# Kernel tuning notes

Measured on AMD Instinct MI355X. Metric: run time of the kernel, lower is better.

## Reference

```python
import jax, jax.numpy as jnp
import numpy as np

# Dims: batch=64, n_cols=512, n_e=80, n_i=20, embed=512
DT_OVER_TAU = 0.1  # leaky rate-neuron integration constant (dt/tau)

B, C, NE, NI, E = 64, 512, 80, 20, 512


def setup_inputs() -> dict:
    key = jax.random.key(0)
    ks = jax.random.split(key, 12)
    return {
        "thal": jax.random.normal(ks[0], (B, E), jnp.float32),
        "thal_increments": jax.random.normal(ks[1], (B, C, E), jnp.float32),
        "l23_fb": jax.random.normal(ks[2], (B, C, NE), jnp.float32),
        # state (rates nonnegative, membrane potentials gaussian)
        "r_e": jax.random.uniform(ks[3], (B, C, NE), jnp.float32),
        "r_i": jax.random.uniform(ks[4], (B, C, NI), jnp.float32),
        "e_v": jax.random.normal(ks[5], (B, C, NE), jnp.float32),
        "i_v": jax.random.normal(ks[6], (B, C, NI), jnp.float32),
        # learned params (per-column weight stacks)
        "input_proj": jax.random.normal(ks[7], (C, NE, E), jnp.float32) * (1.0 / np.sqrt(E).astype(np.float32)),
        "feedback_proj": jax.random.normal(ks[8], (C, NE, NE), jnp.float32) * (1.0 / np.sqrt(NE).astype(np.float32)),
        # static synapses: nonnegative weights, sign handled by E/I convention
        "W_ee": jax.random.uniform(ks[9], (C, NE, NE), jnp.float32) * (1.0 / np.sqrt(NE).astype(np.float32)),
        "W_ei": jax.random.uniform(ks[10], (C, NI, NE), jnp.float32) * (1.0 / np.sqrt(NE).astype(np.float32)),
        "W_ie": jax.random.uniform(ks[11], (C, NE, NI), jnp.float32) * (1.0 / np.sqrt(NI).astype(np.float32)),
    }


def reference(thal, thal_increments, l23_fb, r_e, r_i, e_v, i_v,
              input_proj, feedback_proj, W_ee, W_ei, W_ie):
    # thal [B,E] broadcast over columns + per-column increments -> [B,C,E]
    thal_full = thal[:, None, :] + thal_increments
    # external + feedback drive onto excitatory pop: [B,C,NE]
    I_ext = jnp.einsum('bce,coe->bco', thal_full, input_proj)
    I_fb = jnp.einsum('bce,coe->bco', l23_fb, feedback_proj)
    # synapse currents (static weights; E->E, E->I excitatory, I->E inhibitory)
    I_ee = jnp.einsum('bcp,cop->bco', r_e, W_ee)   # [B,C,NE]
    I_ei = jnp.einsum('bcp,cop->bco', r_e, W_ei)   # [B,C,NI]
    I_ie = -jnp.einsum('bcp,cop->bco', r_i, W_ie)  # [B,C,NE], inhibitory
    I_e_total = I_ext + I_fb + I_ee + I_ie
    I_i_total = I_ei
    # leaky rate-neuron state update: v <- v + dt/tau * (-v + I); r = relu(v)
    v_e_new = e_v + DT_OVER_TAU * (I_e_total - e_v)
    v_i_new = i_v + DT_OVER_TAU * (I_i_total - i_v)
    r_e_new = jax.nn.relu(v_e_new)
    r_i_new = jax.nn.relu(v_i_new)
    # (layer_outputs e_out/l23_out/l5_out all alias r_e_new; return new state too)
    return r_e_new, r_i_new, v_e_new, v_i_new
```

## Files before the change

### kernel.cpp

```cpp
#include <hip/hip_runtime.h>


typedef unsigned int u32;

__global__ __launch_bounds__(256) void ei_cols_f32(
    const float* __restrict__ thal,
    const float* __restrict__ inc,
    const float* __restrict__ l23,
    const float* __restrict__ re_in,
    const float* __restrict__ ri_in,
    const float* __restrict__ ev_in,
    const float* __restrict__ iv_in,
    const float* __restrict__ in_proj,
    const float* __restrict__ fb_proj,
    const float* __restrict__ w_ee,
    const float* __restrict__ w_ei,
    const float* __restrict__ w_ie,
    float* __restrict__ out)
{
  __shared__ __align__(16) float smem[14784];
  const int c = blockIdx.x;
  const int tid = threadIdx.x;
  const int tx = tid & 15;
  const int ty = tid >> 4;

  float acc_e[4][5];
  float acc_i[4][2];
#pragma unroll
  for (int ib = 0; ib < 4; ++ib) {
#pragma unroll
    for (int io = 0; io < 5; ++io) acc_e[ib][io] = 0.f;
    acc_i[ib][0] = 0.f;
    acc_i[ib][1] = 0.f;
  }

  {
    float* As = smem;
    float* Ws = smem + 4352;
    for (int k0 = 0; k0 < 512; k0 += 64) {
      __syncthreads();
      for (int l = tid; l < 1024; l += 256) {
        int b = l >> 4, kk = (l & 15) << 2;
        float4 tv = *(const float4*)(thal + b * 512 + k0 + kk);
        float4 iv = *(const float4*)(inc + (size_t)b * 262144 + (size_t)c * 512 + k0 + kk);
        float4 s;
        s.x = tv.x + iv.x; s.y = tv.y + iv.y; s.z = tv.z + iv.z; s.w = tv.w + iv.w;
        *(float4*)(As + b * 68 + kk) = s;
      }
      for (int l = tid; l < 1280; l += 256) {
        int o = l >> 4, kk = (l & 15) << 2;
        *(float4*)(Ws + o * 68 + kk) =
            *(const float4*)(in_proj + (size_t)c * 40960 + o * 512 + k0 + kk);
      }
      __syncthreads();
#pragma unroll 4
      for (int kc = 0; kc < 64; kc += 4) {
        float4 av[4], wv[5];
#pragma unroll
        for (int ib = 0; ib < 4; ++ib)
          av[ib] = *(const float4*)(As + (ty + 16 * ib) * 68 + kc);
#pragma unroll
        for (int io = 0; io < 5; ++io)
          wv[io] = *(const float4*)(Ws + (tx + 16 * io) * 68 + kc);
#pragma unroll
        for (int ib = 0; ib < 4; ++ib)
#pragma unroll
          for (int io = 0; io < 5; ++io) {
            float a = acc_e[ib][io];
            a = fmaf(av[ib].x, wv[io].x, a);
            a = fmaf(av[ib].y, wv[io].y, a);
            a = fmaf(av[ib].z, wv[io].z, a);
            a = fmaf(av[ib].w, wv[io].w, a);
            acc_e[ib][io] = a;
          }
      }
    }
  }

  {
    __syncthreads();
    float* As = smem;
    float* Bs = smem + 5376;
    for (int l = tid; l < 1280; l += 256) {
      int b = l / 20, kk = (l % 20) << 2;
      *(float4*)(As + b * 84 + kk) =
          *(const float4*)(l23 + ((size_t)b * 512 + c) * 80 + kk);
    }
    for (int l = tid; l < 1600; l += 256) {
      int o = l / 20, kk = (l % 20) << 2;
      *(float4*)(Bs + o * 84 + kk) =
          *(const float4*)(fb_proj + ((size_t)c * 80 + o) * 80 + kk);
    }
    __syncthreads();
#pragma unroll 4
    for (int kc = 0; kc < 80; kc += 4) {
      float4 av[4], wv[5];
#pragma unroll
      for (int ib = 0; ib < 4; ++ib)
        av[ib] = *(const float4*)(As + (ty + 16 * ib) * 84 + kc);
#pragma unroll
      for (int io = 0; io < 5; ++io)
        wv[io] = *(const float4*)(Bs + (tx + 16 * io) * 84 + kc);
#pragma unroll
      for (int ib = 0; ib < 4; ++ib)
#pragma unroll
        for (int io = 0; io < 5; ++io) {
          float a = acc_e[ib][io];
          a = fmaf(av[ib].x, wv[io].x, a);
          a = fmaf(av[ib].y, wv[io].y, a);
          a = fmaf(av[ib].z, wv[io].z, a);
          a = fmaf(av[ib].w, wv[io].w, a);
          acc_e[ib][io] = a;
        }
    }
  }

  {
    __syncthreads();
    float* As = smem;
    float* W1 = smem + 5376;
    float* W2 = smem + 12096;
    for (int l = tid; l < 1280; l += 256) {
      int b = l / 20, kk = (l % 20) << 2;
      *(float4*)(As + b * 84 + kk) =
          *(const float4*)(re_in + ((size_t)b * 512 + c) * 80 + kk);
    }
    for (int l = tid; l < 1600; l += 256) {
      int o = l / 20, kk = (l % 20) << 2;
      *(float4*)(W1 + o * 84 + kk) =
          *(const float4*)(w_ee + ((size_t)c * 80 + o) * 80 + kk);
    }
    for (int l = tid; l < 640; l += 256) {
      int o = l / 20, kk = (l % 20) << 2;
      float4 v = {0.f, 0.f, 0.f, 0.f};
      if (o < 20) v = *(const float4*)(w_ei + ((size_t)c * 20 + o) * 80 + kk);
      *(float4*)(W2 + o * 84 + kk) = v;
    }
    __syncthreads();
#pragma unroll 4
    for (int kc = 0; kc < 80; kc += 4) {
      float4 av[4], wv[5], w2[2];
#pragma unroll
      for (int ib = 0; ib < 4; ++ib)
        av[ib] = *(const float4*)(As + (ty + 16 * ib) * 84 + kc);
#pragma unroll
      for (int io = 0; io < 5; ++io)
        wv[io] = *(const float4*)(W1 + (tx + 16 * io) * 84 + kc);
#pragma unroll
      for (int io = 0; io < 2; ++io)
        w2[io] = *(const float4*)(W2 + (tx + 16 * io) * 84 + kc);
#pragma unroll
      for (int ib = 0; ib < 4; ++ib) {
#pragma unroll
        for (int io = 0; io < 5; ++io) {
          float a = acc_e[ib][io];
          a = fmaf(av[ib].x, wv[io].x, a);
          a = fmaf(av[ib].y, wv[io].y, a);
          a = fmaf(av[ib].z, wv[io].z, a);
          a = fmaf(av[ib].w, wv[io].w, a);
          acc_e[ib][io] = a;
        }
#pragma unroll
        for (int io = 0; io < 2; ++io) {
          float a = acc_i[ib][io];
          a = fmaf(av[ib].x, w2[io].x, a);
          a = fmaf(av[ib].y, w2[io].y, a);
          a = fmaf(av[ib].z, w2[io].z, a);
          a = fmaf(av[ib].w, w2[io].w, a);
          acc_i[ib][io] = a;
        }
      }
    }
  }

  {
    __syncthreads();
    float* Ri = smem;
    float* Wn = smem + 1792;
    for (int l = tid; l < 320; l += 256) {
      int b = l / 5, kk = (l % 5) << 2;
      *(float4*)(Ri + b * 28 + kk) =
          *(const float4*)(ri_in + ((size_t)b * 512 + c) * 20 + kk);
    }
    for (int l = tid; l < 400; l += 256) {
      int o = l / 5, kk = (l % 5) << 2;
      float4 v = *(const float4*)(w_ie + ((size_t)c * 80 + o) * 20 + kk);
      v.x = -v.x; v.y = -v.y; v.z = -v.z; v.w = -v.w;
      *(float4*)(Wn + o * 28 + kk) = v;
    }
    __syncthreads();
#pragma unroll
    for (int kc = 0; kc < 20; kc += 4) {
      float4 av[4], wv[5];
#pragma unroll
      for (int ib = 0; ib < 4; ++ib)
        av[ib] = *(const float4*)(Ri + (ty + 16 * ib) * 28 + kc);
#pragma unroll
      for (int io = 0; io < 5; ++io)
        wv[io] = *(const float4*)(Wn + (tx + 16 * io) * 28 + kc);
#pragma unroll
      for (int ib = 0; ib < 4; ++ib)
#pragma unroll
        for (int io = 0; io < 5; ++io) {
          float a = acc_e[ib][io];
          a = fmaf(av[ib].x, wv[io].x, a);
          a = fmaf(av[ib].y, wv[io].y, a);
          a = fmaf(av[ib].z, wv[io].z, a);
          a = fmaf(av[ib].w, wv[io].w, a);
          acc_e[ib][io] = a;
        }
    }
  }

  const size_t R_ri = 2621440u;
  const size_t R_ve = 3276800u;
  const size_t R_vi = 5898240u;
#pragma unroll
  for (int ib = 0; ib < 4; ++ib) {
    int b = ty + 16 * ib;
#pragma unroll
    for (int io = 0; io < 5; ++io) {
      int o = tx + 16 * io;
      size_t g = ((size_t)b * 512 + c) * 80 + o;
      float ev = ev_in[g];
      float v = ev + 0.1f * (acc_e[ib][io] - ev);
      out[g] = fmaxf(v, 0.f);
      out[R_ve + g] = v;
    }
#pragma unroll
    for (int io = 0; io < 2; ++io) {
      int oi = tx + 16 * io;
      if (oi < 20) {
        size_t g = ((size_t)b * 512 + c) * 20 + oi;
        float iv = iv_in[g];
        float v = iv + 0.1f * (acc_i[ib][io] - iv);
        out[R_ri + g] = fmaxf(v, 0.f);
        out[R_vi + g] = v;
      }
    }
  }
}

extern "C" void kernel_launch(void* const* d_in, const int* in_sizes, int n_in,
                              void* d_out, int out_size, void* d_ws, size_t ws_size,
                              hipStream_t stream) {
  const float* thal = (const float*)d_in[0];
  const float* inc = (const float*)d_in[1];
  const float* l23 = (const float*)d_in[2];
  const float* re = (const float*)d_in[3];
  const float* ri = (const float*)d_in[4];
  const float* ev = (const float*)d_in[5];
  const float* iv = (const float*)d_in[6];
  const float* in_proj = (const float*)d_in[7];
  const float* fb_proj = (const float*)d_in[8];
  const float* w_ee = (const float*)d_in[9];
  const float* w_ei = (const float*)d_in[10];
  const float* w_ie = (const float*)d_in[11];
  float* out = (float*)d_out;
  ei_cols_f32<<<dim3(512), dim3(256), 0, stream>>>(
      thal, inc, l23, re, ri, ev, iv, in_proj, fb_proj, w_ee, w_ei, w_ie, out);
}
```

Before: 307.1 us.

## Switch per-column GEMMs to bf16 MFMA with register-prefetched double buffering

```diff
diff --git a/kernel.cpp b/kernel.cpp
--- a/kernel.cpp
+++ b/kernel.cpp
@@ -1,9 +1,26 @@
 #include <hip/hip_runtime.h>
-
-
+#include <hip/hip_bf16.h>
+
+typedef __attribute__((ext_vector_type(8))) short bf16x8;
+typedef __attribute__((ext_vector_type(4))) float f32x4;
+typedef unsigned short u16;
 typedef unsigned int u32;
 
-__global__ __launch_bounds__(256) void ei_cols_f32(
+__device__ __forceinline__ u16 f2bf(float f) {
+  __hip_bfloat16 h = __float2bfloat16(f);
+  u16 u;
+  __builtin_memcpy(&u, &h, 2);
+  return u;
+}
+__device__ __forceinline__ void cvt4_store(u16* dst, float4 v) {
+  u16 rr[4] = {f2bf(v.x), f2bf(v.y), f2bf(v.z), f2bf(v.w)};
+  uint2 p;
+  __builtin_memcpy(&p, rr, 8);
+  *(uint2*)dst = p;
+}
+
+
+__global__ __launch_bounds__(256) void ei_cols_mfma(
     const float* __restrict__ thal,
     const float* __restrict__ inc,
     const float* __restrict__ l23,
@@ -18,226 +35,248 @@
     const float* __restrict__ w_ie,
     float* __restrict__ out)
 {
-  __shared__ __align__(16) float smem[14784];
+  __shared__ __align__(16) unsigned char smem[41472];
   const int c = blockIdx.x;
   const int tid = threadIdx.x;
-  const int tx = tid & 15;
-  const int ty = tid >> 4;
-
-  float acc_e[4][5];
-  float acc_i[4][2];
-#pragma unroll
-  for (int ib = 0; ib < 4; ++ib) {
-#pragma unroll
-    for (int io = 0; io < 5; ++io) acc_e[ib][io] = 0.f;
-    acc_i[ib][0] = 0.f;
-    acc_i[ib][1] = 0.f;
-  }
+  const int lane = tid & 63;
+  const int wave = tid >> 6;
+  const int nidx = lane & 15;
+  const int quad = lane >> 4;
+  const int m0 = wave * 16;
+
+  f32x4 acc_e[5], acc_i[2];
+#pragma unroll
+  for (int j = 0; j < 5; ++j) acc_e[j] = (f32x4){0.f, 0.f, 0.f, 0.f};
+#pragma unroll
+  for (int j = 0; j < 2; ++j) acc_i[j] = (f32x4){0.f, 0.f, 0.f, 0.f};
 
   {
-    float* As = smem;
-    float* Ws = smem + 4352;
-    for (int k0 = 0; k0 < 512; k0 += 64) {
+    float4 tv[4], gv[4], wv[5];
+
+    auto load_regs = [&](int k0) {
+#pragma unroll
+      for (int j = 0; j < 4; ++j) {
+        int l = tid + j * 256;
+        int b = l >> 4, kk = (l & 15) << 2;
+        tv[j] = *(const float4*)(thal + b * 512 + k0 + kk);
+        gv[j] = *(const float4*)(inc + (size_t)b * 262144 + (size_t)c * 512 + k0 + kk);
+      }
+#pragma unroll
+      for (int j = 0; j < 5; ++j) {
+        int l = tid + j * 256;
+        int o = l >> 4, kk = (l & 15) << 2;
+        wv[j] = *(const float4*)(in_proj + (size_t)c * 40960 + o * 512 + k0 + kk);
+      }
+    };
+    auto store_buf = [&](int p) {
+      u16* A = (u16*)(smem + p * 20736);
+      u16* W = (u16*)(smem + 9216 + p * 20736);
+#pragma unroll
+      for (int j = 0; j < 4; ++j) {
+        int l = tid + j * 256;
+        int b = l >> 4, kk = (l & 15) << 2;
+        float4 s;
+        s.x = tv[j].x + gv[j].x; s.y = tv[j].y + gv[j].y;
+        s.z = tv[j].z + gv[j].z; s.w = tv[j].w + gv[j].w;
+        cvt4_store(A + b * 72 + kk, s);
+      }
+#pragma unroll
+      for (int j = 0; j < 5; ++j) {
+        int l = tid + j * 256;
+        int o = l >> 4, kk = (l & 15) << 2;
+        cvt4_store(W + o * 72 + kk, wv[j]);
+      }
+    };
+
+    load_regs(0);
+    store_buf(0);
+    for (int i = 0; i < 8; ++i) {
       __syncthreads();
-      for (int l = tid; l < 1024; l += 256) {
-        int b = l >> 4, kk = (l & 15) << 2;
-        float4 tv = *(const float4*)(thal + b * 512 + k0 + kk);
-        float4 iv = *(const float4*)(inc + (size_t)b * 262144 + (size_t)c * 512 + k0 + kk);
-        float4 s;
-        s.x = tv.x + iv.x; s.y = tv.y + iv.y; s.z = tv.z + iv.z; s.w = tv.w + iv.w;
-        *(float4*)(As + b * 68 + kk) = s;
-      }
-      for (int l = tid; l < 1280; l += 256) {
-        int o = l >> 4, kk = (l & 15) << 2;
-        *(float4*)(Ws + o * 68 + kk) =
-            *(const float4*)(in_proj + (size_t)c * 40960 + o * 512 + k0 + kk);
-      }
-      __syncthreads();
-#pragma unroll 4
-      for (int kc = 0; kc < 64; kc += 4) {
-        float4 av[4], wv[5];
-#pragma unroll
-        for (int ib = 0; ib < 4; ++ib)
-          av[ib] = *(const float4*)(As + (ty + 16 * ib) * 68 + kc);
-#pragma unroll
-        for (int io = 0; io < 5; ++io)
-          wv[io] = *(const float4*)(Ws + (tx + 16 * io) * 68 + kc);
-#pragma unroll
-        for (int ib = 0; ib < 4; ++ib)
-#pragma unroll
-          for (int io = 0; io < 5; ++io) {
-            float a = acc_e[ib][io];
-            a = fmaf(av[ib].x, wv[io].x, a);
-            a = fmaf(av[ib].y, wv[io].y, a);
-            a = fmaf(av[ib].z, wv[io].z, a);
-            a = fmaf(av[ib].w, wv[io].w, a);
-            acc_e[ib][io] = a;
-          }
-      }
+      if (i < 7) load_regs((i + 1) * 64);
+      const int p = i & 1;
+      u16* A = (u16*)(smem + p * 20736);
+      u16* W = (u16*)(smem + 9216 + p * 20736);
+#pragma unroll
+      for (int kk0 = 0; kk0 < 64; kk0 += 32) {
+        bf16x8 a = *(const bf16x8*)(A + (m0 + nidx) * 72 + kk0 + quad * 8);
+#pragma unroll
+        for (int j = 0; j < 5; ++j) {
+          bf16x8 b = *(const bf16x8*)(W + (j * 16 + nidx) * 72 + kk0 + quad * 8);
+          acc_e[j] = __builtin_amdgcn_mfma_f32_16x16x32_bf16(a, b, acc_e[j], 0, 0, 0);
+        }
+      }
+      if (i < 7) store_buf((i + 1) & 1);
     }
   }
 
   {
     __syncthreads();
-    float* As = smem;
-    float* Bs = smem + 5376;
+    u16* As = (u16*)smem;
+    u16* Bs = (u16*)(smem + 13312);
     for (int l = tid; l < 1280; l += 256) {
       int b = l / 20, kk = (l % 20) << 2;
-      *(float4*)(As + b * 84 + kk) =
-          *(const float4*)(l23 + ((size_t)b * 512 + c) * 80 + kk);
+      cvt4_store(As + b * 104 + kk,
+                 *(const float4*)(l23 + ((size_t)b * 512 + c) * 80 + kk));
+    }
+    for (int l = tid; l < 128; l += 256) {
+      int b = l >> 1, off = 80 + (l & 1) * 8;
+      *(uint4*)(As + b * 104 + off) = (uint4){0u, 0u, 0u, 0u};
     }
     for (int l = tid; l < 1600; l += 256) {
       int o = l / 20, kk = (l % 20) << 2;
-      *(float4*)(Bs + o * 84 + kk) =
-          *(const float4*)(fb_proj + ((size_t)c * 80 + o) * 80 + kk);
-    }
-    __syncthreads();
-#pragma unroll 4
-    for (int kc = 0; kc < 80; kc += 4) {
-      float4 av[4], wv[5];
-#pragma unroll
-      for (int ib = 0; ib < 4; ++ib)
-        av[ib] = *(const float4*)(As + (ty + 16 * ib) * 84 + kc);
-#pragma unroll
-      for (int io = 0; io < 5; ++io)
-        wv[io] = *(const float4*)(Bs + (tx + 16 * io) * 84 + kc);
-#pragma unroll
-      for (int ib = 0; ib < 4; ++ib)
-#pragma unroll
-        for (int io = 0; io < 5; ++io) {
-          float a = acc_e[ib][io];
-          a = fmaf(av[ib].x, wv[io].x, a);
-          a = fmaf(av[ib].y, wv[io].y, a);
-          a = fmaf(av[ib].z, wv[io].z, a);
-          a = fmaf(av[ib].w, wv[io].w, a);
-          acc_e[ib][io] = a;
-        }
+      cvt4_store(Bs + o * 104 + kk,
+                 *(const float4*)(fb_proj + ((size_t)c * 80 + o) * 80 + kk));
+    }
+    for (int l = tid; l < 160; l += 256) {
+      int o = l >> 1, off = 80 + (l & 1) * 8;
+      *(uint4*)(Bs + o * 104 + off) = (uint4){0u, 0u, 0u, 0u};
+    }
+    __syncthreads();
+#pragma unroll
+    for (int kk0 = 0; kk0 < 96; kk0 += 32) {
+      bf16x8 a = *(const bf16x8*)(As + (m0 + nidx) * 104 + kk0 + quad * 8);
+#pragma unroll
+      for (int j = 0; j < 5; ++j) {
+        bf16x8 b = *(const bf16x8*)(Bs + (j * 16 + nidx) * 104 + kk0 + quad * 8);
+        acc_e[j] = __builtin_amdgcn_mfma_f32_16x16x32_bf16(a, b, acc_e[j], 0, 0, 0);
+      }
     }
   }
 
   {
     __syncthreads();
-    float* As = smem;
-    float* W1 = smem + 5376;
-    float* W2 = smem + 12096;
+    u16* As = (u16*)smem;
+    u16* W1 = (u16*)(smem + 13312);
+    u16* W2 = (u16*)(smem + 29952);
     for (int l = tid; l < 1280; l += 256) {
       int b = l / 20, kk = (l % 20) << 2;
-      *(float4*)(As + b * 84 + kk) =
-          *(const float4*)(re_in + ((size_t)b * 512 + c) * 80 + kk);
+      cvt4_store(As + b * 104 + kk,
+                 *(const float4*)(re_in + ((size_t)b * 512 + c) * 80 + kk));
+    }
+    for (int l = tid; l < 128; l += 256) {
+      int b = l >> 1, off = 80 + (l & 1) * 8;
+      *(uint4*)(As + b * 104 + off) = (uint4){0u, 0u, 0u, 0u};
     }
     for (int l = tid; l < 1600; l += 256) {
       int o = l / 20, kk = (l % 20) << 2;
-      *(float4*)(W1 + o * 84 + kk) =
-          *(const float4*)(w_ee + ((size_t)c * 80 + o) * 80 + kk);
-    }
-    for (int l = tid; l < 640; l += 256) {
+      cvt4_store(W1 + o * 104 + kk,
+                 *(const float4*)(w_ee + ((size_t)c * 80 + o) * 80 + kk));
+    }
+    for (int l = tid; l < 160; l += 256) {
+      int o = l >> 1, off = 80 + (l & 1) * 8;
+      *(uint4*)(W1 + o * 104 + off) = (uint4){0u, 0u, 0u, 0u};
+    }
+    for (int l = tid; l < 400; l += 256) {
       int o = l / 20, kk = (l % 20) << 2;
-      float4 v = {0.f, 0.f, 0.f, 0.f};
-      if (o < 20) v = *(const float4*)(w_ei + ((size_t)c * 20 + o) * 80 + kk);
-      *(float4*)(W2 + o * 84 + kk) = v;
-    }
-    __syncthreads();
-#pragma unroll 4
-    for (int kc = 0; kc < 80; kc += 4) {
-      float4 av[4], wv[5], w2[2];
-#pragma unroll
-      for (int ib = 0; ib < 4; ++ib)
-        av[ib] = *(const float4*)(As + (ty + 16 * ib) * 84 + kc);
-#pragma unroll
-      for (int io = 0; io < 5; ++io)
-        wv[io] = *(const float4*)(W1 + (tx + 16 * io) * 84 + kc);
-#pragma unroll
-      for (int io = 0; io < 2; ++io)
-        w2[io] = *(const float4*)(W2 + (tx + 16 * io) * 84 + kc);
-#pragma unroll
-      for (int ib = 0; ib < 4; ++ib) {
-#pragma unroll
-        for (int io = 0; io < 5; ++io) {
-          float a = acc_e[ib][io];
-          a = fmaf(av[ib].x, wv[io].x, a);
-          a = fmaf(av[ib].y, wv[io].y, a);
-          a = fmaf(av[ib].z, wv[io].z, a);
-          a = fmaf(av[ib].w, wv[io].w, a);
-          acc_e[ib][io] = a;
-        }
-#pragma unroll
-        for (int io = 0; io < 2; ++io) {
-          float a = acc_i[ib][io];
-          a = fmaf(av[ib].x, w2[io].x, a);
-          a = fmaf(av[ib].y, w2[io].y, a);
-          a = fmaf(av[ib].z, w2[io].z, a);
-          a = fmaf(av[ib].w, w2[io].w, a);
-          acc_i[ib][io] = a;
-        }
+      cvt4_store(W2 + o * 104 + kk,
+                 *(const float4*)(w_ei + ((size_t)c * 20 + o) * 80 + kk));
+    }
+    for (int l = tid; l < 40; l += 256) {
+      int o = l >> 1, off = 80 + (l & 1) * 8;
+      *(uint4*)(W2 + o * 104 + off) = (uint4){0u, 0u, 0u, 0u};
+    }
+    for (int l = tid; l < 156; l += 256) {
+      int o = 20 + l / 13, off = (l % 13) * 8;
+      *(uint4*)(W2 + o * 104 + off) = (uint4){0u, 0u, 0u, 0u};
+    }
+    __syncthreads();
+#pragma unroll
+    for (int kk0 = 0; kk0 < 96; kk0 += 32) {
+      bf16x8 a = *(const bf16x8*)(As + (m0 + nidx) * 104 + kk0 + quad * 8);
+#pragma unroll
+      for (int j = 0; j < 5; ++j) {
+        bf16x8 b = *(const bf16x8*)(W1 + (j * 16 + nidx) * 104 + kk0 + quad * 8);
+        acc_e[j] = __builtin_amdgcn_mfma_f32_16x16x32_bf16(a, b, acc_e[j], 0, 0, 0);
+      }
+#pragma unroll
+      for (int j = 0; j < 2; ++j) {
+        bf16x8 b = *(const bf16x8*)(W2 + (j * 16 + nidx) * 104 + kk0 + quad * 8);
+        acc_i[j] = __builtin_amdgcn_mfma_f32_16x16x32_bf16(a, b, acc_i[j], 0, 0, 0);
       }
     }
   }
 
   {
     __syncthreads();
-    float* Ri = smem;
-    float* Wn = smem + 1792;
+    u16* Ri = (u16*)smem;
+    u16* Wn = (u16*)(smem + 5120);
     for (int l = tid; l < 320; l += 256) {
       int b = l / 5, kk = (l % 5) << 2;
-      *(float4*)(Ri + b * 28 + kk) =
-          *(const float4*)(ri_in + ((size_t)b * 512 + c) * 20 + kk);
+      cvt4_store(Ri + b * 40 + kk,
+                 *(const float4*)(ri_in + ((size_t)b * 512 + c) * 20 + kk));
+    }
+    for (int l = tid; l < 192; l += 256) {
+      int b = l / 3, kk = 20 + (l % 3) * 4;
+      *(uint2*)(Ri + b * 40 + kk) = (uint2){0u, 0u};
     }
     for (int l = tid; l < 400; l += 256) {
       int o = l / 5, kk = (l % 5) << 2;
       float4 v = *(const float4*)(w_ie + ((size_t)c * 80 + o) * 20 + kk);
       v.x = -v.x; v.y = -v.y; v.z = -v.z; v.w = -v.w;
-      *(float4*)(Wn + o * 28 + kk) = v;
-    }
-    __syncthreads();
-#pragma unroll
-    for (int kc = 0; kc < 20; kc += 4) {
-      float4 av[4], wv[5];
-#pragma unroll
-      for (int ib = 0; ib < 4; ++ib)
-        av[ib] = *(const float4*)(Ri + (ty + 16 * ib) * 28 + kc);
-#pragma unroll
-      for (int io = 0; io < 5; ++io)
-        wv[io] = *(const float4*)(Wn + (tx + 16 * io) * 28 + kc);
-#pragma unroll
-      for (int ib = 0; ib < 4; ++ib)
-#pragma unroll
-        for (int io = 0; io < 5; ++io) {
-          float a = acc_e[ib][io];
-          a = fmaf(av[ib].x, wv[io].x, a);
-          a = fmaf(av[ib].y, wv[io].y, a);
-          a = fmaf(av[ib].z, wv[io].z, a);
-          a = fmaf(av[ib].w, wv[io].w, a);
-          acc_e[ib][io] = a;
-        }
-    }
-  }
+      cvt4_store(Wn + o * 40 + kk, v);
+    }
+    for (int l = tid; l < 240; l += 256) {
+      int o = l / 3, kk = 20 + (l % 3) * 4;
+      *(uint2*)(Wn + o * 40 + kk) = (uint2){0u, 0u};
+    }
+    __syncthreads();
+    {
+      bf16x8 a = *(const bf16x8*)(Ri + (m0 + nidx) * 40 + quad * 8);
+#pragma unroll
+      for (int j = 0; j < 5; ++j) {
+        bf16x8 b = *(const bf16x8*)(Wn + (j * 16 + nidx) * 40 + quad * 8);
+        acc_e[j] = __builtin_amdgcn_mfma_f32_16x16x32_bf16(a, b, acc_e[j], 0, 0, 0);
+      }
+    }
+  }
+
+  __syncthreads();
+  float* aE = (float*)smem;
+  float* aI = (float*)(smem + 21504);
+#pragma unroll
+  for (int j = 0; j < 5; ++j)
+#pragma unroll
+    for (int r = 0; r < 4; ++r)
+      aE[(m0 + quad * 4 + r) * 84 + j * 16 + nidx] = acc_e[j][r];
+#pragma unroll
+  for (int j = 0; j < 2; ++j) {
+    int col = j * 16 + nidx;
+    if (col < 20) {
+#pragma unroll
+      for (int r = 0; r < 4; ++r)
+        aI[(m0 + quad * 4 + r) * 36 + col] = acc_i[j][r];
+    }
+  }
+  __syncthreads();
 
   const size_t R_ri = 2621440u;
   const size_t R_ve = 3276800u;
   const size_t R_vi = 5898240u;
-#pragma unroll
-  for (int ib = 0; ib < 4; ++ib) {
-    int b = ty + 16 * ib;
-#pragma unroll
-    for (int io = 0; io < 5; ++io) {
-      int o = tx + 16 * io;
-      size_t g = ((size_t)b * 512 + c) * 80 + o;
-      float ev = ev_in[g];
-      float v = ev + 0.1f * (acc_e[ib][io] - ev);
-      out[g] = fmaxf(v, 0.f);
-      out[R_ve + g] = v;
-    }
-#pragma unroll
-    for (int io = 0; io < 2; ++io) {
-      int oi = tx + 16 * io;
-      if (oi < 20) {
-        size_t g = ((size_t)b * 512 + c) * 20 + oi;
-        float iv = iv_in[g];
-        float v = iv + 0.1f * (acc_i[ib][io] - iv);
-        out[R_ri + g] = fmaxf(v, 0.f);
-        out[R_vi + g] = v;
-      }
-    }
+  for (int l = tid; l < 1280; l += 256) {
+    int b = l / 20, c2 = (l % 20) << 2;
+    float4 a = *(const float4*)(aE + b * 84 + c2);
+    size_t g = ((size_t)b * 512 + c) * 80 + c2;
+    float4 ev = *(const float4*)(ev_in + g);
+    float4 v, r;
+    v.x = ev.x + 0.1f * (a.x - ev.x); r.x = fmaxf(v.x, 0.f);
+    v.y = ev.y + 0.1f * (a.y - ev.y); r.y = fmaxf(v.y, 0.f);
+    v.z = ev.z + 0.1f * (a.z - ev.z); r.z = fmaxf(v.z, 0.f);
+    v.w = ev.w + 0.1f * (a.w - ev.w); r.w = fmaxf(v.w, 0.f);
+    *(float4*)(out + g) = r;
+    *(float4*)(out + R_ve + g) = v;
+  }
+  for (int l = tid; l < 320; l += 256) {
+    int b = l / 5, c2 = (l % 5) << 2;
+    float4 a = *(const float4*)(aI + b * 36 + c2);
+    size_t g = ((size_t)b * 512 + c) * 20 + c2;
+    float4 iv = *(const float4*)(iv_in + g);
+    float4 v, r;
+    v.x = iv.x + 0.1f * (a.x - iv.x); r.x = fmaxf(v.x, 0.f);
+    v.y = iv.y + 0.1f * (a.y - iv.y); r.y = fmaxf(v.y, 0.f);
+    v.z = iv.z + 0.1f * (a.z - iv.z); r.z = fmaxf(v.z, 0.f);
+    v.w = iv.w + 0.1f * (a.w - iv.w); r.w = fmaxf(v.w, 0.f);
+    *(float4*)(out + R_ri + g) = r;
+    *(float4*)(out + R_vi + g) = v;
   }
 }
 
@@ -257,6 +296,6 @@
   const float* w_ei = (const float*)d_in[10];
   const float* w_ie = (const float*)d_in[11];
   float* out = (float*)d_out;
-  ei_cols_f32<<<dim3(512), dim3(256), 0, stream>>>(
+  ei_cols_mfma<<<dim3(512), dim3(256), 0, stream>>>(
       thal, inc, l23, re, ri, ev, iv, in_proj, fb_proj, w_ee, w_ei, w_ie, out);
 }
```

New measurement: 257.9 us. -16.0%, faster.
